# Kernel optimization log

Hardware: AMD Instinct MI355X
Metric: run time of the kernel (lower is better)

Reference implementation:

```python
import jax, jax.numpy as jnp
import numpy as np

VOXEL_SIZE = 0.04
M = 32768            # voxels surviving from previous level
V = 9                # views per fragment
C = 24               # image feature channels at finest scale
H, W = 120, 160      # fine feature map size (640x480 images /4)
C_PRE = 50           # channels[1] + tsdf + occ from previous level
UP_OFFSETS = np.array([[0,0,0,0],[0,1,0,0],[0,0,1,0],[0,0,0,1],
                       [0,1,1,0],[0,1,0,1],[0,0,1,1],[0,1,1,1]], dtype=np.int32)


def setup_inputs():
    key = jax.random.key(0)
    ks = jax.random.split(key, 10)
    pre_feat = jax.random.normal(ks[0], (M, C_PRE), jnp.float32)
    xyz = jax.random.randint(ks[1], (M, 3), 0, 94).astype(jnp.int32)
    pre_coords = jnp.concatenate([jnp.zeros((M, 1), jnp.int32), xyz], axis=1)
    feats = jax.random.normal(ks[2], (V, 1, C, H, W), jnp.float32)
    # plausible pinhole KRcam = K @ [R|t], identity rotation, jittered translation
    fx = fy = 100.0
    cx, cy = (W - 1) / 2.0, (H - 1) / 2.0
    K = np.array([[fx, 0, cx, 0], [0, fy, cy, 0], [0, 0, 1, 0], [0, 0, 0, 1]], np.float32)
    t = np.asarray(jax.random.uniform(ks[3], (V, 3), minval=-0.2, maxval=0.2))
    RT = np.tile(np.eye(4, dtype=np.float32), (V, 1, 1))
    RT[:, :3, 3] = t
    KRcam = jnp.asarray(np.einsum('ij,vjk->vik', K, RT).astype(np.float32))[:, None]  # (V,1,4,4)
    vol_origin = jnp.array([[-1.9, -1.9, 0.5]], jnp.float32)
    w2ac = jnp.asarray(np.eye(4, dtype=np.float32)[None]) + 0.01 * jax.random.normal(ks[4], (1, 4, 4), jnp.float32)
    W_sp = jax.random.normal(ks[5], (C + 1 + C_PRE, 24), jnp.float32) * 0.1
    b_sp = jnp.zeros((24,), jnp.float32)
    W_t = jax.random.normal(ks[6], (24, 1), jnp.float32) * 0.1
    b_t = jnp.zeros((1,), jnp.float32)
    W_o = jax.random.normal(ks[7], (24, 1), jnp.float32) * 0.1
    b_o = jnp.zeros((1,), jnp.float32)
    return dict(pre_feat=pre_feat, pre_coords=pre_coords, feats=feats, KRcam=KRcam,
                vol_origin=vol_origin, world_to_aligned_camera=w2ac,
                W_sp=W_sp, b_sp=b_sp, W_t=W_t, b_t=b_t, W_o=W_o, b_o=b_o)


def upsample(pre_feat, pre_coords, interval):
    # 1 -> 8 octree coordinate upsample (NeuConHead.upsample)
    off = jnp.asarray(UP_OFFSETS) * interval          # batch col stays 0
    up_coords = (pre_coords[:, None, :] + off[None]).reshape(-1, 4)
    up_feat = jnp.broadcast_to(pre_feat[:, None, :], (pre_feat.shape[0], 8, pre_feat.shape[1])).reshape(-1, pre_feat.shape[1])
    return up_feat, up_coords


def back_project(coords_xyz, origin, voxel_size, feats, KRcam):
    # coords_xyz: (N,3) int voxel coords; feats: (V,C,H,W); KRcam: (V,4,4)
    n = coords_xyz.shape[0]
    world = coords_xyz.astype(jnp.float32) * voxel_size + origin          # (N,3)
    homog = jnp.concatenate([world, jnp.ones((n, 1), jnp.float32)], 1)    # (N,4)
    im_p = jnp.einsum('vij,nj->vin', KRcam, homog)                        # (V,4,N)
    im_x, im_y, im_z = im_p[:, 0], im_p[:, 1], im_p[:, 2]
    safe_z = jnp.where(jnp.abs(im_z) > 1e-9, im_z, 1e-9)
    px = im_x / safe_z
    py = im_y / safe_z
    mask = (px >= 0) & (px <= W - 1) & (py >= 0) & (py <= H - 1) & (im_z > 0)  # (V,N)

    def sample_view(img, x, y, m):
        # bilinear grid_sample, align_corners=True, zero padding; img (C,H,W)
        x0 = jnp.floor(x); y0 = jnp.floor(y)
        wx = x - x0; wy = y - y0
        def gather(xi, yi):
            ok = (xi >= 0) & (xi < W) & (yi >= 0) & (yi < H)
            v = img[:, jnp.clip(yi, 0, H - 1).astype(jnp.int32), jnp.clip(xi, 0, W - 1).astype(jnp.int32)]
            return v * ok  # (C,N)
        top = gather(x0, y0) * (1 - wx) + gather(x0 + 1, y0) * wx
        bot = gather(x0, y0 + 1) * (1 - wx) + gather(x0 + 1, y0 + 1) * wx
        return jnp.where(m, top * (1 - wy) + bot * wy, 0.0)  # (C,N)

    fsamp = jax.vmap(sample_view)(feats, px, py, mask)        # (V,C,N)
    zed = jnp.where(mask, im_z, 0.0)                          # (V,N)
    count = mask.sum(0).astype(jnp.float32)                   # (N,)
    denom = jnp.maximum(count, 1.0)
    features = fsamp.sum(0) / denom                           # (C,N)
    z = zed.sum(0) / denom                                    # (N,)
    pos = z > 0
    npos = jnp.maximum(pos.sum(), 1).astype(jnp.float32)
    zmean = jnp.where(pos, z, 0.0).sum() / npos
    znorm = jnp.sqrt(jnp.where(pos, (z - zmean) ** 2, 0.0).sum()) + 1e-5  # torch.norm
    zn = jnp.where(pos, (z - zmean) / znorm, 0.0)
    volume = jnp.concatenate([features.T, zn[:, None]], axis=1)  # (N, C+1)
    return volume, count


def reference(pre_feat, feats, KRcam, vol_origin, world_to_aligned_camera,
              W_sp, b_sp, W_t, b_t, W_o, b_o, pre_coords):
    up_feat, up_coords = upsample(pre_feat, pre_coords, 1)
    volume, count = back_project(up_coords[:, 1:], vol_origin[0], VOXEL_SIZE,
                                 feats[:, 0], KRcam[:, 0])
    feat = jnp.concatenate([volume, up_feat], axis=1)          # (N, 75)
    # r_coords: world -> aligned camera frame (bs=1)
    world = up_coords[:, 1:].astype(jnp.float32) * VOXEL_SIZE + vol_origin[0]
    homog = jnp.concatenate([world, jnp.ones_like(world[:, :1])], axis=1)
    cam = homog @ world_to_aligned_camera[0, :3, :].T          # (N,3)
    r_coords = jnp.concatenate([cam, up_coords[:, :1].astype(jnp.float32)], axis=1)
    h = jax.nn.relu(feat @ W_sp + b_sp)                        # SPVCNN stand-in head
    tsdf = h @ W_t + b_t
    occ = h @ W_o + b_o
    out = jnp.concatenate([tsdf, occ], axis=1)                 # (N,2)
    return out, count, r_coords
```

## Files before the change

### kernel.cpp

```cpp
#include <hip/hip_runtime.h>
#include <hip/hip_fp16.h>

#define Mpts 32768
#define Vv 9
#define Cc 24
#define Hh 120
#define Ww 160
#define Npts (Mpts * 8)
#define PIX (Hh * Ww)
#define VOXEL 0.04f

#define NB_TF   (Vv * 300)
#define NB_GEMM (Mpts / 256)
#define NB_Z    (Npts / 256)

#define OFF_TF    32768
#define OFF_PREH  (OFF_TF + Vv * PIX * 32)

typedef __attribute__((ext_vector_type(2))) float f32x2;
typedef __attribute__((ext_vector_type(4))) float f32x4;
typedef __attribute__((ext_vector_type(4))) int i32x4;

__device__ __forceinline__ unsigned pack4fp8(float a, float b, float c,
                                             float d) {
  int u = __builtin_amdgcn_cvt_pk_fp8_f32(a, b, 0, false);
  u = __builtin_amdgcn_cvt_pk_fp8_f32(c, d, u, true);
  return (unsigned)u;
}

__global__ __launch_bounds__(256) void prep_kernel(
    const float* __restrict__ feats, const float* __restrict__ pre_feat,
    const float* __restrict__ W_sp, const float* __restrict__ b_sp,
    const int* __restrict__ pre_coords, const float* __restrict__ KRcam,
    const float* __restrict__ vol_origin, uint4* __restrict__ tf,
    float* __restrict__ pre_h, double* __restrict__ red) {
  __shared__ float tile[64][Cc + 1];
  __shared__ float Wl[50 * Cc];
  __shared__ float bl[Cc];
  __shared__ float KRs[Vv * 12];
  __shared__ float origs[3];
  __shared__ float redl[3][4];
  int blk = blockIdx.x;

  if (blk < NB_TF) {
    int v = blk / 300;
    int p0 = (blk % 300) * 64;
    const float* src = feats + (size_t)v * (Cc * PIX);
    for (int i = threadIdx.x; i < Cc * 64; i += 256) {
      int c = i >> 6, p = i & 63;
      tile[p][c] = __builtin_nontemporal_load(src + c * PIX + p0 + p);
    }
    __syncthreads();
    uint4* dst = tf + ((size_t)v * PIX + p0) * 2;
    if (threadIdx.x < 128) {
      int p = threadIdx.x >> 1, sel = threadIdx.x & 1;
      const float* t = &tile[p][0];
      uint4 u;
      if (sel == 0) {
        u.x = pack4fp8(t[0], t[1], t[2], t[3]);
        u.y = pack4fp8(t[4], t[5], t[6], t[7]);
        u.z = pack4fp8(t[8], t[9], t[10], t[11]);
        u.w = pack4fp8(t[12], t[13], t[14], t[15]);
      } else {
        u.x = pack4fp8(t[16], t[17], t[18], t[19]);
        u.y = pack4fp8(t[20], t[21], t[22], t[23]);
        u.z = 0;
        u.w = 0;
      }
      dst[p * 2 + sel] = u;
    }
  } else if (blk < NB_TF + NB_GEMM) {
    int mb = blk - NB_TF;
    for (int i = threadIdx.x; i < 50 * Cc; i += 256) Wl[i] = W_sp[25 * Cc + i];
    if (threadIdx.x < Cc) bl[threadIdx.x] = b_sp[threadIdx.x];
    __syncthreads();
    int m = mb * 256 + threadIdx.x;
    float acc[Cc];
#pragma unroll
    for (int j = 0; j < Cc; j++) acc[j] = bl[j];
    const f32x2* pf = (const f32x2*)(pre_feat + (size_t)m * 50);
#pragma unroll 5
    for (int k = 0; k < 25; k++) {
      f32x2 x = __builtin_nontemporal_load(pf + k);
#pragma unroll
      for (int j = 0; j < Cc; j++)
        acc[j] += x.x * Wl[(2 * k) * Cc + j] + x.y * Wl[(2 * k + 1) * Cc + j];
    }
    f32x4* o4 = (f32x4*)(pre_h + (size_t)m * Cc);
#pragma unroll
    for (int t = 0; t < 6; t++) {
      f32x4 v4 = {acc[4 * t], acc[4 * t + 1], acc[4 * t + 2], acc[4 * t + 3]};
      o4[t] = v4;
    }
  } else {
    int zblk = blk - (NB_TF + NB_GEMM);
    for (int i = threadIdx.x; i < Vv * 12; i += 256) {
      int v = i / 12, r = i - v * 12;
      KRs[i] = KRcam[v * 16 + r];
    }
    if (threadIdx.x < 3) origs[threadIdx.x] = vol_origin[threadIdx.x];
    __syncthreads();
    int n = zblk * 256 + threadIdx.x;
    int m = n >> 3, o = n & 7;
    i32x4 pc = __builtin_nontemporal_load((const i32x4*)pre_coords + m);
    int cx = pc.y + ((0xB2 >> o) & 1);
    int cy = pc.z + ((0xD4 >> o) & 1);
    int cz = pc.w + ((0xE8 >> o) & 1);
    float wx0 = (float)cx * VOXEL + origs[0];
    float wy0 = (float)cy * VOXEL + origs[1];
    float wz0 = (float)cz * VOXEL + origs[2];
    float zsum = 0.f;
    int cnt = 0;
    for (int v = 0; v < Vv; v++) {
      const float* kr = &KRs[v * 12];
      float ix = kr[0] * wx0 + kr[1] * wy0 + kr[2] * wz0 + kr[3];
      float iy = kr[4] * wx0 + kr[5] * wy0 + kr[6] * wz0 + kr[7];
      float iz = kr[8] * wx0 + kr[9] * wy0 + kr[10] * wz0 + kr[11];
      float sz = (fabsf(iz) > 1e-9f) ? iz : 1e-9f;
      float px = ix / sz;
      float py = iy / sz;
      bool msk = (px >= 0.f) && (px <= (float)(Ww - 1)) && (py >= 0.f) &&
                 (py <= (float)(Hh - 1)) && (iz > 0.f);
      if (msk) {
        zsum += iz;
        cnt++;
      }
    }
    float denom = fmaxf((float)cnt, 1.f);
    float z = zsum / denom;
    float rz = (z > 0.f) ? z : 0.f;
    float rz2 = rz * rz;
    float rcn = (z > 0.f) ? 1.f : 0.f;
#pragma unroll
    for (int off = 32; off > 0; off >>= 1) {
      rz += __shfl_down(rz, off);
      rz2 += __shfl_down(rz2, off);
      rcn += __shfl_down(rcn, off);
    }
    int wid = threadIdx.x >> 6, lid = threadIdx.x & 63;
    if (lid == 0) {
      redl[0][wid] = rz;
      redl[1][wid] = rz2;
      redl[2][wid] = rcn;
    }
    __syncthreads();
    if (threadIdx.x == 0) {
      float a = 0.f, b = 0.f, c = 0.f;
#pragma unroll
      for (int w = 0; w < 4; w++) {
        a += redl[0][w];
        b += redl[1][w];
        c += redl[2][w];
      }
      double* r3 = red + (size_t)zblk * 3;
      r3[0] = (double)a;
      r3[1] = (double)b;
      r3[2] = (double)c;
    }
  }
}

__device__ __forceinline__ void acc16(uint4 A, float w, float* acc) {
#pragma unroll
  for (int t = 0; t < 4; t++) {
    unsigned u = ((const unsigned*)&A)[t];
    f32x2 f0 = __builtin_amdgcn_cvt_pk_f32_fp8((int)u, false);
    f32x2 f1 = __builtin_amdgcn_cvt_pk_f32_fp8((int)u, true);
    acc[4 * t + 0] += w * f0.x;
    acc[4 * t + 1] += w * f0.y;
    acc[4 * t + 2] += w * f1.x;
    acc[4 * t + 3] += w * f1.y;
  }
}
__device__ __forceinline__ void acc8v(unsigned ux, unsigned uy, float w,
                                      float* acc) {
  f32x2 f0 = __builtin_amdgcn_cvt_pk_f32_fp8((int)ux, false);
  f32x2 f1 = __builtin_amdgcn_cvt_pk_f32_fp8((int)ux, true);
  f32x2 f2 = __builtin_amdgcn_cvt_pk_f32_fp8((int)uy, false);
  f32x2 f3 = __builtin_amdgcn_cvt_pk_f32_fp8((int)uy, true);
  acc[0] += w * f0.x;
  acc[1] += w * f0.y;
  acc[2] += w * f1.x;
  acc[3] += w * f1.y;
  acc[4] += w * f2.x;
  acc[5] += w * f2.y;
  acc[6] += w * f3.x;
  acc[7] += w * f3.y;
}

__global__ __launch_bounds__(256) void main_kernel(
    const int* __restrict__ pre_coords, const uint4* __restrict__ tfq,
    const float* __restrict__ KRcam, const float* __restrict__ vol_origin,
    const float* __restrict__ w2ac, const float* __restrict__ W_sp,
    const float* __restrict__ W_t, const float* __restrict__ b_t,
    const float* __restrict__ W_o, const float* __restrict__ b_o,
    const float* __restrict__ pre_h, float* __restrict__ out,
    const double* __restrict__ red) {
  __shared__ float KR[Vv * 12];
  __shared__ float w2a[12];
  __shared__ float orig[3];
  __shared__ double dredl[3][4];
  __shared__ float s_zmean, s_izn;
  for (int i = threadIdx.x; i < Vv * 12; i += 256) {
    int v = i / 12, r = i - v * 12;
    KR[i] = KRcam[v * 16 + r];
  }
  if (threadIdx.x < 12) w2a[threadIdx.x] = w2ac[threadIdx.x];
  if (threadIdx.x < 3) orig[threadIdx.x] = vol_origin[threadIdx.x];

  {
    double a = 0.0, b = 0.0, c = 0.0;
    for (int s = threadIdx.x; s < NB_Z; s += 256) {
      const double* r3 = red + (size_t)s * 3;
      a += r3[0];
      b += r3[1];
      c += r3[2];
    }
#pragma unroll
    for (int off = 32; off > 0; off >>= 1) {
      a += __shfl_down(a, off);
      b += __shfl_down(b, off);
      c += __shfl_down(c, off);
    }
    int wid = threadIdx.x >> 6, lid = threadIdx.x & 63;
    if (lid == 0) {
      dredl[0][wid] = a;
      dredl[1][wid] = b;
      dredl[2][wid] = c;
    }
    __syncthreads();
    if (threadIdx.x == 0) {
      double A = 0.0, B = 0.0, C = 0.0;
#pragma unroll
      for (int w = 0; w < 4; w++) {
        A += dredl[0][w];
        B += dredl[1][w];
        C += dredl[2][w];
      }
      double npos = (C > 0.0) ? C : 1.0;
      double zmean = A / npos;
      double var = B - 2.0 * zmean * A + C * zmean * zmean;
      if (var < 0.0) var = 0.0;
      double znorm = sqrt(var) + 1e-5;
      s_zmean = (float)zmean;
      s_izn = (float)(1.0 / znorm);
    }
  }
  __syncthreads();

  int n = blockIdx.x * 256 + threadIdx.x;
  int m = n >> 3, o = n & 7;
  i32x4 pc = __builtin_nontemporal_load((const i32x4*)pre_coords + m);
  int cx = pc.y + ((0xB2 >> o) & 1);
  int cy = pc.z + ((0xD4 >> o) & 1);
  int cz = pc.w + ((0xE8 >> o) & 1);
  float wx0 = (float)cx * VOXEL + orig[0];
  float wy0 = (float)cy * VOXEL + orig[1];
  float wz0 = (float)cz * VOXEL + orig[2];

  {
    float camx = w2a[0] * wx0 + w2a[1] * wy0 + w2a[2] * wz0 + w2a[3];
    float camy = w2a[4] * wx0 + w2a[5] * wy0 + w2a[6] * wz0 + w2a[7];
    float camz = w2a[8] * wx0 + w2a[9] * wy0 + w2a[10] * wz0 + w2a[11];
    f32x4 rc = {camx, camy, camz, (float)pc.x};
    __builtin_nontemporal_store(rc, (f32x4*)(out + 3 * (size_t)Npts) + n);
  }

  float acc[Cc];
#pragma unroll
  for (int c = 0; c < Cc; c++) acc[c] = 0.f;
  float zsum = 0.f;
  int cnt = 0;

  for (int v = 0; v < Vv; v++) {
    const float* kr = &KR[v * 12];
    float ix = kr[0] * wx0 + kr[1] * wy0 + kr[2] * wz0 + kr[3];
    float iy = kr[4] * wx0 + kr[5] * wy0 + kr[6] * wz0 + kr[7];
    float iz = kr[8] * wx0 + kr[9] * wy0 + kr[10] * wz0 + kr[11];
    float sz = (fabsf(iz) > 1e-9f) ? iz : 1e-9f;
    float px = ix / sz;
    float py = iy / sz;
    bool msk = (px >= 0.f) && (px <= (float)(Ww - 1)) && (py >= 0.f) &&
               (py <= (float)(Hh - 1)) && (iz > 0.f);
    if (msk) {
      int x0 = (int)floorf(px), y0 = (int)floorf(py);
      int xs = min(x0, Ww - 2), ys = min(y0, Hh - 2);
      float wx = px - (float)xs, wy = py - (float)ys;
      float w00 = (1.f - wx) * (1.f - wy);
      float w10 = wx * (1.f - wy);
      float w01 = (1.f - wx) * wy;
      float w11 = wx * wy;
      const uint4* p = tfq + ((size_t)(v * PIX + ys * Ww + xs)) * 2;
      const uint4* q = p + Ww * 2;
      uint4 A = p[0], B = p[2], C = q[0], D = q[2];
      uint2 Ab = *(const uint2*)(p + 1), Bb = *(const uint2*)(p + 3);
      uint2 Cb = *(const uint2*)(q + 1), Db = *(const uint2*)(q + 3);
      acc16(A, w00, &acc[0]);
      acc8v(Ab.x, Ab.y, w00, &acc[16]);
      acc16(B, w10, &acc[0]);
      acc8v(Bb.x, Bb.y, w10, &acc[16]);
      acc16(C, w01, &acc[0]);
      acc8v(Cb.x, Cb.y, w01, &acc[16]);
      acc16(D, w11, &acc[0]);
      acc8v(Db.x, Db.y, w11, &acc[16]);
      zsum += iz;
      cnt++;
    }
  }

  float denom = fmaxf((float)cnt, 1.f);
  float invd = 1.f / denom;
  float z = zsum * invd;

  float h[Cc];
  {
    const f32x4* ph4 = (const f32x4*)(pre_h + (size_t)m * Cc);
#pragma unroll
    for (int t = 0; t < 6; t++) {
      f32x4 v4 = ph4[t];
      h[4 * t + 0] = v4.x;
      h[4 * t + 1] = v4.y;
      h[4 * t + 2] = v4.z;
      h[4 * t + 3] = v4.w;
    }
  }
#pragma unroll
  for (int c = 0; c < Cc; c++) {
    float f = acc[c] * invd;
#pragma unroll
    for (int j = 0; j < Cc; j++) h[j] += f * W_sp[c * Cc + j];
  }

  float zn = (z > 0.f) ? (z - s_zmean) * s_izn : 0.f;
  float tsdf = b_t[0], occ = b_o[0];
#pragma unroll
  for (int j = 0; j < Cc; j++) {
    float hj = fmaxf(h[j] + zn * W_sp[24 * Cc + j], 0.f);
    tsdf += hj * W_t[j];
    occ += hj * W_o[j];
  }
  f32x2 o2 = {tsdf, occ};
  __builtin_nontemporal_store(o2, (f32x2*)out + n);
  __builtin_nontemporal_store((float)cnt, out + 2 * (size_t)Npts + n);
}

extern "C" void kernel_launch(void* const* d_in, const int* in_sizes, int n_in,
                              void* d_out, int out_size, void* d_ws,
                              size_t ws_size, hipStream_t stream) {
  const float* pre_feat = (const float*)d_in[0];
  const int* pre_coords = (const int*)d_in[1];
  const float* feats = (const float*)d_in[2];
  const float* KRcam = (const float*)d_in[3];
  const float* vol_origin = (const float*)d_in[4];
  const float* w2ac = (const float*)d_in[5];
  const float* W_sp = (const float*)d_in[6];
  const float* b_sp = (const float*)d_in[7];
  const float* W_t = (const float*)d_in[8];
  const float* b_t = (const float*)d_in[9];
  const float* W_o = (const float*)d_in[10];
  const float* b_o = (const float*)d_in[11];

  float* out = (float*)d_out;
  char* ws = (char*)d_ws;
  double* red = (double*)ws;
  uint4* tf = (uint4*)(ws + OFF_TF);
  float* pre_h = (float*)(ws + OFF_PREH);

  prep_kernel<<<NB_TF + NB_GEMM + NB_Z, 256, 0, stream>>>(
      feats, pre_feat, W_sp, b_sp, pre_coords, KRcam, vol_origin, tf, pre_h,
      red);
  main_kernel<<<NB_Z, 256, 0, stream>>>(pre_coords, tf, KRcam, vol_origin,
                                        w2ac, W_sp, W_t, b_t, W_o, b_o, pre_h,
                                        out, red);
}
```

Baseline: 141.5 us.

## Split fp8 feature table into 16B+8B planes and precompute z-stats in prep

Splits the packed fp8 feature table into a 16-byte plane for channels 0-15 and a separate 8-byte plane for channels 16-23. This removes the 8 bytes of padding per pixel and lets two adjacent pixels' tail channels load as one 16-byte read. The global z-mean/norm reduction moves from every main_kernel block into the last-finishing prep block, found with an atomic ticket counter. This removes a redundant 1024-entry double reduction per main block, at the cost of an extra memset launch and a serialized tail in prep.

```diff
diff --git a/kernel.cpp b/kernel.cpp
--- a/kernel.cpp
+++ b/kernel.cpp
@@ -14,12 +14,21 @@
 #define NB_GEMM (Mpts / 256)
 #define NB_Z    (Npts / 256)
 
-#define OFF_TF    32768
-#define OFF_PREH  (OFF_TF + Vv * PIX * 32)
+#define OFF_RED   0
+#define OFF_TICK  24576
+#define OFF_ZST   24640
+#define OFF_TF16  32768
+#define OFF_TF8   (OFF_TF16 + Vv * PIX * 16)
+#define OFF_PREH  (OFF_TF8 + Vv * PIX * 8)
 
 typedef __attribute__((ext_vector_type(2))) float f32x2;
 typedef __attribute__((ext_vector_type(4))) float f32x4;
 typedef __attribute__((ext_vector_type(4))) int i32x4;
+
+__device__ __forceinline__ uint4 ld_u4_a8(const void* p) {
+  struct __attribute__((packed, aligned(8))) A8 { uint4 v; };
+  return ((const A8*)p)->v;
+}
 
 __device__ __forceinline__ unsigned pack4fp8(float a, float b, float c,
                                              float d) {
@@ -32,14 +41,18 @@
     const float* __restrict__ feats, const float* __restrict__ pre_feat,
     const float* __restrict__ W_sp, const float* __restrict__ b_sp,
     const int* __restrict__ pre_coords, const float* __restrict__ KRcam,
-    const float* __restrict__ vol_origin, uint4* __restrict__ tf,
-    float* __restrict__ pre_h, double* __restrict__ red) {
+    const float* __restrict__ vol_origin, uint4* __restrict__ tf16,
+    uint2* __restrict__ tf8, float* __restrict__ pre_h,
+    double* __restrict__ red, int* __restrict__ tick,
+    float* __restrict__ zst) {
   __shared__ float tile[64][Cc + 1];
   __shared__ float Wl[50 * Cc];
   __shared__ float bl[Cc];
   __shared__ float KRs[Vv * 12];
   __shared__ float origs[3];
   __shared__ float redl[3][4];
+  __shared__ double dredl[3][4];
+  __shared__ int s_last;
   int blk = blockIdx.x;
 
   if (blk < NB_TF) {
@@ -51,23 +64,22 @@
       tile[p][c] = __builtin_nontemporal_load(src + c * PIX + p0 + p);
     }
     __syncthreads();
-    uint4* dst = tf + ((size_t)v * PIX + p0) * 2;
-    if (threadIdx.x < 128) {
-      int p = threadIdx.x >> 1, sel = threadIdx.x & 1;
+    if (threadIdx.x < 64) {
+      int p = threadIdx.x;
       const float* t = &tile[p][0];
       uint4 u;
-      if (sel == 0) {
-        u.x = pack4fp8(t[0], t[1], t[2], t[3]);
-        u.y = pack4fp8(t[4], t[5], t[6], t[7]);
-        u.z = pack4fp8(t[8], t[9], t[10], t[11]);
-        u.w = pack4fp8(t[12], t[13], t[14], t[15]);
-      } else {
-        u.x = pack4fp8(t[16], t[17], t[18], t[19]);
-        u.y = pack4fp8(t[20], t[21], t[22], t[23]);
-        u.z = 0;
-        u.w = 0;
-      }
-      dst[p * 2 + sel] = u;
+      u.x = pack4fp8(t[0], t[1], t[2], t[3]);
+      u.y = pack4fp8(t[4], t[5], t[6], t[7]);
+      u.z = pack4fp8(t[8], t[9], t[10], t[11]);
+      u.w = pack4fp8(t[12], t[13], t[14], t[15]);
+      tf16[(size_t)v * PIX + p0 + p] = u;
+    } else if (threadIdx.x < 128) {
+      int p = threadIdx.x - 64;
+      const float* t = &tile[p][0];
+      uint2 u;
+      u.x = pack4fp8(t[16], t[17], t[18], t[19]);
+      u.y = pack4fp8(t[20], t[21], t[22], t[23]);
+      tf8[(size_t)v * PIX + p0 + p] = u;
     }
   } else if (blk < NB_TF + NB_GEMM) {
     int mb = blk - NB_TF;
@@ -156,6 +168,48 @@
       r3[0] = (double)a;
       r3[1] = (double)b;
       r3[2] = (double)c;
+      __threadfence();
+      int t = atomicAdd(tick, 1);
+      s_last = (t == NB_Z - 1) ? 1 : 0;
+    }
+    __syncthreads();
+    if (s_last) {
+      __threadfence();
+      double a = 0.0, b = 0.0, c = 0.0;
+      for (int s = threadIdx.x; s < NB_Z; s += 256) {
+        const double* r3 = red + (size_t)s * 3;
+        a += r3[0];
+        b += r3[1];
+        c += r3[2];
+      }
+#pragma unroll
+      for (int off = 32; off > 0; off >>= 1) {
+        a += __shfl_down(a, off);
+        b += __shfl_down(b, off);
+        c += __shfl_down(c, off);
+      }
+      if (lid == 0) {
+        dredl[0][wid] = a;
+        dredl[1][wid] = b;
+        dredl[2][wid] = c;
+      }
+      __syncthreads();
+      if (threadIdx.x == 0) {
+        double A = 0.0, B = 0.0, C = 0.0;
+#pragma unroll
+        for (int w = 0; w < 4; w++) {
+          A += dredl[0][w];
+          B += dredl[1][w];
+          C += dredl[2][w];
+        }
+        double npos = (C > 0.0) ? C : 1.0;
+        double zmean = A / npos;
+        double var = B - 2.0 * zmean * A + C * zmean * zmean;
+        if (var < 0.0) var = 0.0;
+        double znorm = sqrt(var) + 1e-5;
+        zst[0] = (float)zmean;
+        zst[1] = (float)(1.0 / znorm);
+      }
     }
   }
 }
@@ -189,64 +243,26 @@
 }
 
 __global__ __launch_bounds__(256) void main_kernel(
-    const int* __restrict__ pre_coords, const uint4* __restrict__ tfq,
-    const float* __restrict__ KRcam, const float* __restrict__ vol_origin,
-    const float* __restrict__ w2ac, const float* __restrict__ W_sp,
-    const float* __restrict__ W_t, const float* __restrict__ b_t,
-    const float* __restrict__ W_o, const float* __restrict__ b_o,
-    const float* __restrict__ pre_h, float* __restrict__ out,
-    const double* __restrict__ red) {
+    const int* __restrict__ pre_coords, const uint4* __restrict__ tf16,
+    const unsigned char* __restrict__ tf8, const float* __restrict__ KRcam,
+    const float* __restrict__ vol_origin, const float* __restrict__ w2ac,
+    const float* __restrict__ W_sp, const float* __restrict__ W_t,
+    const float* __restrict__ b_t, const float* __restrict__ W_o,
+    const float* __restrict__ b_o, const float* __restrict__ pre_h,
+    float* __restrict__ out, const float* __restrict__ zst) {
   __shared__ float KR[Vv * 12];
   __shared__ float w2a[12];
   __shared__ float orig[3];
-  __shared__ double dredl[3][4];
-  __shared__ float s_zmean, s_izn;
   for (int i = threadIdx.x; i < Vv * 12; i += 256) {
     int v = i / 12, r = i - v * 12;
     KR[i] = KRcam[v * 16 + r];
   }
   if (threadIdx.x < 12) w2a[threadIdx.x] = w2ac[threadIdx.x];
   if (threadIdx.x < 3) orig[threadIdx.x] = vol_origin[threadIdx.x];
-
-  {
-    double a = 0.0, b = 0.0, c = 0.0;
-    for (int s = threadIdx.x; s < NB_Z; s += 256) {
-      const double* r3 = red + (size_t)s * 3;
-      a += r3[0];
-      b += r3[1];
-      c += r3[2];
-    }
-#pragma unroll
-    for (int off = 32; off > 0; off >>= 1) {
-      a += __shfl_down(a, off);
-      b += __shfl_down(b, off);
-      c += __shfl_down(c, off);
-    }
-    int wid = threadIdx.x >> 6, lid = threadIdx.x & 63;
-    if (lid == 0) {
-      dredl[0][wid] = a;
-      dredl[1][wid] = b;
-      dredl[2][wid] = c;
-    }
-    __syncthreads();
-    if (threadIdx.x == 0) {
-      double A = 0.0, B = 0.0, C = 0.0;
-#pragma unroll
-      for (int w = 0; w < 4; w++) {
-        A += dredl[0][w];
-        B += dredl[1][w];
-        C += dredl[2][w];
-      }
-      double npos = (C > 0.0) ? C : 1.0;
-      double zmean = A / npos;
-      double var = B - 2.0 * zmean * A + C * zmean * zmean;
-      if (var < 0.0) var = 0.0;
-      double znorm = sqrt(var) + 1e-5;
-      s_zmean = (float)zmean;
-      s_izn = (float)(1.0 / znorm);
-    }
-  }
   __syncthreads();
+
+  float s_zmean = zst[0];
+  float s_izn = zst[1];
 
   int n = blockIdx.x * 256 + threadIdx.x;
   int m = n >> 3, o = n & 7;
@@ -290,19 +306,21 @@
       float w10 = wx * (1.f - wy);
       float w01 = (1.f - wx) * wy;
       float w11 = wx * wy;
-      const uint4* p = tfq + ((size_t)(v * PIX + ys * Ww + xs)) * 2;
-      const uint4* q = p + Ww * 2;
-      uint4 A = p[0], B = p[2], C = q[0], D = q[2];
-      uint2 Ab = *(const uint2*)(p + 1), Bb = *(const uint2*)(p + 3);
-      uint2 Cb = *(const uint2*)(q + 1), Db = *(const uint2*)(q + 3);
+      size_t pp = (size_t)(v * PIX + ys * Ww + xs);
+      const uint4* h16 = tf16 + pp;
+      uint4 A = h16[0], B = h16[1];
+      uint4 C = h16[Ww], D = h16[Ww + 1];
+      const unsigned char* t8 = tf8 + pp * 8;
+      uint4 Tab = ld_u4_a8(t8);
+      uint4 Tcd = ld_u4_a8(t8 + Ww * 8);
       acc16(A, w00, &acc[0]);
-      acc8v(Ab.x, Ab.y, w00, &acc[16]);
       acc16(B, w10, &acc[0]);
-      acc8v(Bb.x, Bb.y, w10, &acc[16]);
       acc16(C, w01, &acc[0]);
-      acc8v(Cb.x, Cb.y, w01, &acc[16]);
       acc16(D, w11, &acc[0]);
-      acc8v(Db.x, Db.y, w11, &acc[16]);
+      acc8v(Tab.x, Tab.y, w00, &acc[16]);
+      acc8v(Tab.z, Tab.w, w10, &acc[16]);
+      acc8v(Tcd.x, Tcd.y, w01, &acc[16]);
+      acc8v(Tcd.z, Tcd.w, w11, &acc[16]);
       zsum += iz;
       cnt++;
     }
@@ -362,14 +380,18 @@
 
   float* out = (float*)d_out;
   char* ws = (char*)d_ws;
-  double* red = (double*)ws;
-  uint4* tf = (uint4*)(ws + OFF_TF);
+  double* red = (double*)(ws + OFF_RED);
+  int* tick = (int*)(ws + OFF_TICK);
+  float* zst = (float*)(ws + OFF_ZST);
+  uint4* tf16 = (uint4*)(ws + OFF_TF16);
+  uint2* tf8 = (uint2*)(ws + OFF_TF8);
   float* pre_h = (float*)(ws + OFF_PREH);
 
+  hipMemsetAsync(ws + OFF_TICK, 0, 64, stream);
   prep_kernel<<<NB_TF + NB_GEMM + NB_Z, 256, 0, stream>>>(
-      feats, pre_feat, W_sp, b_sp, pre_coords, KRcam, vol_origin, tf, pre_h,
-      red);
-  main_kernel<<<NB_Z, 256, 0, stream>>>(pre_coords, tf, KRcam, vol_origin,
-                                        w2ac, W_sp, W_t, b_t, W_o, b_o, pre_h,
-                                        out, red);
-}
+      feats, pre_feat, W_sp, b_sp, pre_coords, KRcam, vol_origin, tf16, tf8,
+      pre_h, red, tick, zst);
+  main_kernel<<<NB_Z, 256, 0, stream>>>(
+      pre_coords, tf16, (const unsigned char*)tf8, KRcam, vol_origin, w2ac,
+      W_sp, W_t, b_t, W_o, b_o, pre_h, out, zst);
+}
```

New measurement: 170.4 us. 1.2x slower.
